# Kernel tuning notes

Hardware: AMD Instinct MI355X
Metric: run time of the kernel (lower is better)

Reference implementation:

```python
import jax, jax.numpy as jnp
import numpy as np

DIM = 1024
HEADS = 16
HDIM = DIM // HEADS
HIDDEN = 4 * DIM
SCALE = HDIM ** -0.5


def layernorm(x, g, b, eps=1e-5):
    mu = jnp.mean(x, axis=-1, keepdims=True)
    var = jnp.var(x, axis=-1, keepdims=True)
    return (x - mu) * jax.lax.rsqrt(var + eps) * g + b


def setup_inputs() -> dict:
    key = jax.random.key(0)
    ks = jax.random.split(key, 8)
    s = 0.02
    return {
        "x": jax.random.normal(ks[0], (4, 1024, DIM), dtype=jnp.float32),
        "ln1_g": jnp.ones((DIM,), jnp.float32),
        "ln1_b": jnp.zeros((DIM,), jnp.float32),
        "ln2_g": jnp.ones((DIM,), jnp.float32),
        "ln2_b": jnp.zeros((DIM,), jnp.float32),
        "qkv_w": jax.random.normal(ks[1], (DIM, 3 * DIM), jnp.float32) * s,
        "qkv_b": jnp.zeros((3 * DIM,), jnp.float32),
        "proj_w": jax.random.normal(ks[2], (DIM, DIM), jnp.float32) * s,
        "proj_b": jnp.zeros((DIM,), jnp.float32),
        "fc1_w": jax.random.normal(ks[3], (DIM, HIDDEN), jnp.float32) * s,
        "fc1_b": jnp.zeros((HIDDEN,), jnp.float32),
        "fc2_w": jax.random.normal(ks[4], (HIDDEN, DIM), jnp.float32) * s,
        "fc2_b": jnp.zeros((DIM,), jnp.float32),
    }


def reference(x, ln1_g, ln1_b, ln2_g, ln2_b, qkv_w, qkv_b, proj_w, proj_b,
              fc1_w, fc1_b, fc2_w, fc2_b):
    B, N, C = x.shape
    # --- attention branch ---
    h = layernorm(x, ln1_g, ln1_b)
    qkv = h @ qkv_w + qkv_b                       # [B,N,3C]
    qkv = qkv.reshape(B, N, 3, HEADS, HDIM)
    q, k, v = jnp.moveaxis(qkv, 2, 0)             # each [B,N,H,Dh]
    q = jnp.swapaxes(q, 1, 2)                      # [B,H,N,Dh]
    k = jnp.swapaxes(k, 1, 2)
    v = jnp.swapaxes(v, 1, 2)
    attn = jnp.einsum('bhqd,bhkd->bhqk', q, k) * SCALE
    attn = jax.nn.softmax(attn, axis=-1)
    o = jnp.einsum('bhqk,bhkd->bhqd', attn, v)     # [B,H,N,Dh]
    o = jnp.swapaxes(o, 1, 2).reshape(B, N, C)
    x = x + (o @ proj_w + proj_b)
    # --- MLP branch ---
    h = layernorm(x, ln2_g, ln2_b)
    h = jax.nn.gelu(h @ fc1_w + fc1_b, approximate=False)
    x = x + (h @ fc2_w + fc2_b)
    return x
```

## Files before the change

kernel.cpp:

```cpp
#include <hip/hip_runtime.h>
#include <math.h>

#define DIM    1024
#define HEADS  16
#define HDIM   64
#define HIDDEN 4096
#define BATCH  4
#define SEQ    1024
#define ROWS   (BATCH * SEQ)

typedef short s16x8 __attribute__((ext_vector_type(8)));
typedef float f32x4 __attribute__((ext_vector_type(4)));

__device__ __forceinline__ float blo(unsigned int u) {
    union { unsigned int i; float f; } x; x.i = u << 16; return x.f;
}
__device__ __forceinline__ float bhi(unsigned int u) {
    union { unsigned int i; float f; } x; x.i = u & 0xffff0000u; return x.f;
}
__device__ __forceinline__ unsigned short f2b(float f) {
    union { float f; unsigned int i; } x; x.f = f;
    unsigned int r = x.i + 0x7fffu + ((x.i >> 16) & 1u);
    return (unsigned short)(r >> 16);
}

__device__ __forceinline__ float gelu_f(float x) {
    float z  = fabsf(x) * 0.70710678118f;
    float t  = __builtin_amdgcn_rcpf(__builtin_fmaf(0.3275911f, z, 1.0f));
    float p  = ((((1.061405429f * t - 1.453152027f) * t + 1.421413741f) * t
                 - 0.284496736f) * t + 0.254829592f) * t;
    float e  = exp2f(-0.72134752f * x * x);
    float w  = 0.5f * p * e;
    float phi = (x >= 0.0f) ? (1.0f - w) : w;
    return x * phi;
}

__device__ __forceinline__ size_t tidx(int row, int k, int Kdim) {
    return ((size_t)(row >> 4) * (Kdim >> 5) + (k >> 5)) * 512
         + (size_t)(((k & 31) >> 3) * 128 + (row & 15) * 8 + (k & 7));
}

__device__ __forceinline__ void gload_lds16(const void* g, void* l) {
    __builtin_amdgcn_global_load_lds(
        (const __attribute__((address_space(1))) unsigned int*)g,
        (__attribute__((address_space(3))) unsigned int*)l, 16, 0, 0);
}

__global__ __launch_bounds__(256) void ln_kernel(const float* __restrict__ x,
                                                 const float* __restrict__ g,
                                                 const float* __restrict__ b,
                                                 unsigned short* __restrict__ out) {
    int row = blockIdx.x;
    const float* xr = x + (size_t)row * DIM;
    int t = threadIdx.x;
    float4 v = *((const float4*)(xr + t * 4));
    float s  = v.x + v.y + v.z + v.w;
    float ss = v.x * v.x + v.y * v.y + v.z * v.z + v.w * v.w;
    __shared__ float red1[256], red2[256];
    red1[t] = s; red2[t] = ss;
    __syncthreads();
    for (int off = 128; off > 0; off >>= 1) {
        if (t < off) { red1[t] += red1[t + off]; red2[t] += red2[t + off]; }
        __syncthreads();
    }
    float mu   = red1[0] * (1.0f / DIM);
    float var  = red2[0] * (1.0f / DIM) - mu * mu;
    float rstd = rsqrtf(var + 1e-5f);
    float4 gv = *((const float4*)(g + t * 4));
    float4 bv = *((const float4*)(b + t * 4));
    ushort4 o;
    o.x = f2b((v.x - mu) * rstd * gv.x + bv.x);
    o.y = f2b((v.y - mu) * rstd * gv.y + bv.y);
    o.z = f2b((v.z - mu) * rstd * gv.z + bv.z);
    o.w = f2b((v.w - mu) * rstd * gv.w + bv.w);
    *((ushort4*)(out + tidx(row, t * 4, DIM))) = o;
}

__global__ __launch_bounds__(256) void reduce_ln(const unsigned short* __restrict__ p0,
                                                 const unsigned short* __restrict__ p1,
                                                 const float* __restrict__ x,
                                                 const float* __restrict__ bias,
                                                 const float* __restrict__ g,
                                                 const float* __restrict__ b,
                                                 float* __restrict__ xout,
                                                 unsigned short* __restrict__ lnout) {
    int row = blockIdx.x;
    int t = threadIdx.x;
    size_t i = (size_t)row * DIM + t * 4;
    float4 xv = *((const float4*)(x + i));
    float4 bi = *((const float4*)(bias + t * 4));
    uint2 w0 = *((const uint2*)(p0 + i));
    uint2 w1 = *((const uint2*)(p1 + i));
    float4 v;
    v.x = xv.x + bi.x + blo(w0.x) + blo(w1.x);
    v.y = xv.y + bi.y + bhi(w0.x) + bhi(w1.x);
    v.z = xv.z + bi.z + blo(w0.y) + blo(w1.y);
    v.w = xv.w + bi.w + bhi(w0.y) + bhi(w1.y);
    *((float4*)(xout + i)) = v;

    float s  = v.x + v.y + v.z + v.w;
    float ss = v.x * v.x + v.y * v.y + v.z * v.z + v.w * v.w;
    __shared__ float red1[256], red2[256];
    red1[t] = s; red2[t] = ss;
    __syncthreads();
    for (int off = 128; off > 0; off >>= 1) {
        if (t < off) { red1[t] += red1[t + off]; red2[t] += red2[t + off]; }
        __syncthreads();
    }
    float mu   = red1[0] * (1.0f / DIM);
    float var  = red2[0] * (1.0f / DIM) - mu * mu;
    float rstd = rsqrtf(var + 1e-5f);
    float4 gv = *((const float4*)(g + t * 4));
    float4 bv = *((const float4*)(b + t * 4));
    ushort4 o;
    o.x = f2b((v.x - mu) * rstd * gv.x + bv.x);
    o.y = f2b((v.y - mu) * rstd * gv.y + bv.y);
    o.z = f2b((v.z - mu) * rstd * gv.z + bv.z);
    o.w = f2b((v.w - mu) * rstd * gv.w + bv.w);
    *((ushort4*)(lnout + tidx(row, t * 4, DIM))) = o;
}

__global__ __launch_bounds__(256) void wconv_t(const float* __restrict__ W,
                                               unsigned short* __restrict__ Wt,
                                               int K, int N) {
    __shared__ unsigned short T[64][68];
    int t = threadIdx.x;
    int n0 = blockIdx.x * 64, k0 = blockIdx.y * 64;
    int cr = t >> 4;
    int cc = (t & 15) * 4;
    #pragma unroll
    for (int r = 0; r < 4; ++r) {
        int kk = cr + 16 * r;
        float4 v = *((const float4*)(W + (size_t)(k0 + kk) * N + n0 + cc));
        T[cc + 0][kk] = f2b(v.x);
        T[cc + 1][kk] = f2b(v.y);
        T[cc + 2][kk] = f2b(v.z);
        T[cc + 3][kk] = f2b(v.w);
    }
    __syncthreads();
    {
        int nn = t >> 2;
        int kg = (t & 3) * 16;
        #pragma unroll
        for (int p = 0; p < 2; ++p) {
            int k8 = kg + p * 8;
            ushort4 lo = *((ushort4*)&T[nn][k8]);
            ushort4 hi = *((ushort4*)&T[nn][k8 + 4]);
            unsigned short* dst = Wt + tidx(n0 + nn, k0 + k8, K);
            *((ushort4*)dst)       = lo;
            *((ushort4*)(dst + 4)) = hi;
        }
    }
}

__global__ __launch_bounds__(256, 4) void mfma_gemm(const unsigned short* __restrict__ A,
                                                 const unsigned short* __restrict__ Bt,
                                                 const float* __restrict__ bias,
                                                 const float* __restrict__ add,
                                                 void* __restrict__ Cout,
                                                 unsigned short* __restrict__ vt,
                                                 unsigned short* __restrict__ p0,
                                                 unsigned short* __restrict__ p1,
                                                 unsigned short* __restrict__ p2,
                                                 unsigned short* __restrict__ p3,
                                                 int M, int N, int K, int Ksplit, int fuse) {
    __shared__ __align__(16) short Asm[8192];
    __shared__ __align__(16) short Bsm[8192];

    const int tid  = threadIdx.x;
    const int lane = tid & 63;
    const int wave = tid >> 6;
    const int wy = wave >> 1, wx = wave & 1;
    const int lr = lane & 15;
    const int lq = lane >> 4;

    int m_t, n_t;
    {
        const int mt = gridDim.x, ntl = gridDim.y, G = 8;
        if (ntl > G) {
            int lin = blockIdx.y * mt + blockIdx.x;
            int gsz = mt * G;
            int grp = lin / gsz;
            int rem = lin - grp * gsz;
            m_t = rem % mt;
            n_t = grp * G + rem / mt;
        } else { m_t = blockIdx.x; n_t = blockIdx.y; }
    }
    const int m0 = m_t * 128, n0 = n_t * 128;
    const int kbase = blockIdx.z * Ksplit;
    const int kch = K >> 5;

    f32x4 acc[4][4];
    #pragma unroll
    for (int i = 0; i < 4; ++i)
        #pragma unroll
        for (int j = 0; j < 4; ++j)
            acc[i][j] = (f32x4){0.f, 0.f, 0.f, 0.f};

    const unsigned short* ag[4]; const unsigned short* bg[4];
    short* al[4]; short* bl[4];
    #pragma unroll
    for (int j = 0; j < 4; ++j) {
        int cid = wave * 4 + j;
        int mb  = cid >> 1;
        int kc  = cid & 1;
        ag[j] = A  + ((size_t)((m0 >> 4) + mb) * kch + (kbase >> 5) + kc) * 512 + lane * 8;
        bg[j] = Bt + ((size_t)((n0 >> 4) + mb) * kch + (kbase >> 5) + kc) * 512 + lane * 8;
        al[j] = &Asm[cid * 512];
        bl[j] = &Bsm[cid * 512];
    }

    for (int k0 = 0; k0 < Ksplit; k0 += 64) {
        #pragma unroll
        for (int j = 0; j < 4; ++j) {
            gload_lds16(ag[j], al[j]);
            gload_lds16(bg[j], bl[j]);
            ag[j] += 1024; bg[j] += 1024;
        }
        __syncthreads();
        #pragma unroll
        for (int kc = 0; kc < 2; ++kc) {
            s16x8 af[4], bf[4];
            #pragma unroll
            for (int i = 0; i < 4; ++i)
                af[i] = *((const s16x8*)&Asm[((wy * 4 + i) * 2 + kc) * 512 + lane * 8]);
            #pragma unroll
            for (int j = 0; j < 4; ++j)
                bf[j] = *((const s16x8*)&Bsm[((wx * 4 + j) * 2 + kc) * 512 + lane * 8]);
            #pragma unroll
            for (int i = 0; i < 4; ++i)
                #pragma unroll
                for (int j = 0; j < 4; ++j)
                    acc[i][j] = __builtin_amdgcn_mfma_f32_16x16x32_bf16(af[i], bf[j], acc[i][j], 0, 0, 0);
        }
        __syncthreads();
    }

    unsigned short* P = nullptr;
    if (fuse == 3) {
        int z = blockIdx.z;
        P = (z == 0) ? p0 : (z == 1) ? p1 : (z == 2) ? p2 : p3;
    }

    #pragma unroll
    for (int j = 0; j < 4; ++j) {
        int col = n0 + wx * 64 + j * 16 + lr;
        float bi = (fuse == 3) ? 0.f : bias[col];
        #pragma unroll
        for (int i = 0; i < 4; ++i) {
            int row0 = m0 + wy * 64 + i * 16 + lq * 4;
            #pragma unroll
            for (int r = 0; r < 4; ++r) {
                float val = acc[i][j][r] + bi;
                int row = row0 + r;
                if (fuse == 3) {
                    P[(size_t)row * N + col] = f2b(val);
                } else if (fuse == 2) {
                    size_t idx = (size_t)row * N + col;
                    ((float*)Cout)[idx] = val + add[idx];
                } else {
                    if (fuse == 1)
                        val = gelu_f(val);
                    unsigned short hv = f2b(val);
                    if (fuse == 0 && vt && col >= 2 * DIM) {
                        int b_ = row >> 10, tok = row & 1023;
                        int hd = col - 2 * DIM, h_ = hd >> 6, d = hd & 63;
                        size_t o = (size_t)(b_ * 16 + h_) * 65536
                                 + ((size_t)(d >> 4) * 32 + (tok >> 5)) * 512
                                 + ((tok & 31) >> 3) * 128 + (d & 15) * 8 + (tok & 7);
                        vt[o] = hv;
                    } else {
                        ((unsigned short*)Cout)[tidx(row, col, N)] = hv;
                    }
                }
            }
        }
    }
}

__global__ __launch_bounds__(256) void reduce_kernel(const unsigned short* __restrict__ p0,
                                                     const unsigned short* __restrict__ p1,
                                                     const unsigned short* __restrict__ p2,
                                                     const unsigned short* __restrict__ p3,
                                                     int S,
                                                     const float* __restrict__ x,
                                                     const float* __restrict__ bias,
                                                     float* __restrict__ out) {
    int i = (blockIdx.x * 256 + threadIdx.x) * 8;
    int col = i & (DIM - 1);
    float4 b0 = *((const float4*)(bias + col));
    float4 b1 = *((const float4*)(bias + col + 4));
    float4 x0 = *((const float4*)(x + i));
    float4 x1 = *((const float4*)(x + i + 4));
    float a[8] = {x0.x + b0.x, x0.y + b0.y, x0.z + b0.z, x0.w + b0.w,
                  x1.x + b1.x, x1.y + b1.y, x1.z + b1.z, x1.w + b1.w};
    const unsigned short* ps[4] = {p0, p1, p2, p3};
    for (int s = 0; s < S; ++s) {
        uint4 w = *((const uint4*)(ps[s] + i));
        a[0] += blo(w.x); a[1] += bhi(w.x);
        a[2] += blo(w.y); a[3] += bhi(w.y);
        a[4] += blo(w.z); a[5] += bhi(w.z);
        a[6] += blo(w.w); a[7] += bhi(w.w);
    }
    *((float4*)(out + i))     = make_float4(a[0], a[1], a[2], a[3]);
    *((float4*)(out + i + 4)) = make_float4(a[4], a[5], a[6], a[7]);
}

__global__ __launch_bounds__(256) void fattn_mfma(const unsigned short* __restrict__ qkv,
                                                  const unsigned short* __restrict__ Vt,
                                                  unsigned short* __restrict__ out) {
    __shared__ __align__(16) short Qs[8192];
    __shared__ __align__(16) short Ks[4096];
    __shared__ __align__(16) short Vs[4096];
    __shared__ __align__(16) short Ps[128 * 72];
    __shared__ __align__(16) short OnesB[512];

    const int tid = threadIdx.x, lane = tid & 63, wave = tid >> 6;
    const int lr = lane & 15, lq = lane >> 4;
    const int L = blockIdx.x;
    const int bh = (L & 7) + 8 * (L >> 6);
    const int b = bh >> 4, h = bh & 15;
    const int q0 = ((L >> 3) & 7) * 128;

    {
        s16x8 z = (s16x8){0,0,0,0,0,0,0,0};
        if (lr == 0) { z[0] = (short)0x3F80; z[1] = (short)0x3F80;
                       z[2] = (short)0x3F80; z[3] = (short)0x3F80;
                       z[4] = (short)0x3F80; z[5] = (short)0x3F80;
                       z[6] = (short)0x3F80; z[7] = (short)0x3F80; }
        if (wave == 0) *((s16x8*)&OnesB[lane * 8]) = z;
    }

    #pragma unroll
    for (int j = 0; j < 4; ++j) {
        int cid = wave * 4 + j;
        const unsigned short* g = qkv + ((size_t)(((b * SEQ + q0) >> 4) + (cid >> 1)) * 96
                                         + 2 * h + (cid & 1)) * 512 + lane * 8;
        gload_lds16(g, &Qs[cid * 512]);
    }

    const unsigned short* kg_[2]; const unsigned short* vg_[2];
    short *kl_[2], *vl_[2];
    #pragma unroll
    for (int j = 0; j < 2; ++j) {
        int cid = wave * 2 + j;
        kg_[j] = qkv + ((size_t)(((b * SEQ) >> 4) + (cid >> 1)) * 96
                        + 32 + 2 * h + (cid & 1)) * 512 + lane * 8;
        vg_[j] = Vt + (size_t)bh * 65536
                 + ((size_t)(cid >> 1) * 32 + (cid & 1)) * 512 + lane * 8;
        kl_[j] = &Ks[cid * 512];
        vl_[j] = &Vs[cid * 512];
    }

    f32x4 osum[2][5];
    #pragma unroll
    for (int i = 0; i < 2; ++i)
        #pragma unroll
        for (int d = 0; d < 5; ++d)
            osum[i][d] = (f32x4){0.f, 0.f, 0.f, 0.f};

    const float c = 0.125f * 1.44269504f;

    for (int k0 = 0; k0 < SEQ; k0 += 64) {
        #pragma unroll
        for (int j = 0; j < 2; ++j) {
            gload_lds16(kg_[j], kl_[j]);
            gload_lds16(vg_[j], vl_[j]);
            kg_[j] += 4 * 96 * 512;
            vg_[j] += 1024;
        }
        __syncthreads();

        f32x4 s[2][4];
        #pragma unroll
        for (int i = 0; i < 2; ++i)
            #pragma unroll
            for (int jb = 0; jb < 4; ++jb)
                s[i][jb] = (f32x4){0.f, 0.f, 0.f, 0.f};
        #pragma unroll
        for (int kc = 0; kc < 2; ++kc) {
            s16x8 aq0 = *((const s16x8*)&Qs[(wave * 4 + 0 + kc) * 512 + lane * 8]);
            s16x8 aq1 = *((const s16x8*)&Qs[(wave * 4 + 2 + kc) * 512 + lane * 8]);
            #pragma unroll
            for (int jb = 0; jb < 4; ++jb) {
                s16x8 bk = *((const s16x8*)&Ks[(jb * 2 + kc) * 512 + lane * 8]);
                s[0][jb] = __builtin_amdgcn_mfma_f32_16x16x32_bf16(aq0, bk, s[0][jb], 0, 0, 0);
                s[1][jb] = __builtin_amdgcn_mfma_f32_16x16x32_bf16(aq1, bk, s[1][jb], 0, 0, 0);
            }
        }

        #pragma unroll
        for (int i = 0; i < 2; ++i)
            #pragma unroll
            for (int r = 0; r < 4; ++r) {
                int prow = (wave * 2 + i) * 16 + lq * 4 + r;
                #pragma unroll
                for (int jb = 0; jb < 4; ++jb)
                    Ps[prow * 72 + jb * 16 + lr] = (short)f2b(exp2f(s[i][jb][r] * c));
            }

        #pragma unroll
        for (int kc = 0; kc < 2; ++kc) {
            s16x8 ap0 = *((const s16x8*)&Ps[((wave * 2 + 0) * 16 + lr) * 72 + kc * 32 + lq * 8]);
            s16x8 ap1 = *((const s16x8*)&Ps[((wave * 2 + 1) * 16 + lr) * 72 + kc * 32 + lq * 8]);
            #pragma unroll
            for (int db = 0; db < 4; ++db) {
                s16x8 bv = *((const s16x8*)&Vs[(db * 2 + kc) * 512 + lane * 8]);
                osum[0][db] = __builtin_amdgcn_mfma_f32_16x16x32_bf16(ap0, bv, osum[0][db], 0, 0, 0);
                osum[1][db] = __builtin_amdgcn_mfma_f32_16x16x32_bf16(ap1, bv, osum[1][db], 0, 0, 0);
            }
            s16x8 bo = *((const s16x8*)&OnesB[lane * 8]);
            osum[0][4] = __builtin_amdgcn_mfma_f32_16x16x32_bf16(ap0, bo, osum[0][4], 0, 0, 0);
            osum[1][4] = __builtin_amdgcn_mfma_f32_16x16x32_bf16(ap1, bo, osum[1][4], 0, 0, 0);
        }
        __syncthreads();
    }

    #pragma unroll
    for (int i = 0; i < 2; ++i) {
        int qrow = q0 + (wave * 2 + i) * 16 + lq * 4;
        #pragma unroll
        for (int r = 0; r < 4; ++r) {
            float lsum = __shfl(osum[i][4][r], lane & 48, 64);
            float inv = 1.0f / lsum;
            int row = b * SEQ + qrow + r;
            #pragma unroll
            for (int db = 0; db < 4; ++db)
                out[tidx(row, h * 64 + db * 16 + lr, DIM)] = f2b(osum[i][db][r] * inv);
        }
    }
}

extern "C" void kernel_launch(void* const* d_in, const int* in_sizes, int n_in,
                              void* d_out, int out_size, void* d_ws, size_t ws_size,
                              hipStream_t stream) {
    const float* x      = (const float*)d_in[0];
    const float* ln1_g  = (const float*)d_in[1];
    const float* ln1_b  = (const float*)d_in[2];
    const float* ln2_g  = (const float*)d_in[3];
    const float* ln2_b  = (const float*)d_in[4];
    const float* qkv_w  = (const float*)d_in[5];
    const float* qkv_b  = (const float*)d_in[6];
    const float* proj_w = (const float*)d_in[7];
    const float* proj_b = (const float*)d_in[8];
    const float* fc1_w  = (const float*)d_in[9];
    const float* fc1_b  = (const float*)d_in[10];
    const float* fc2_w  = (const float*)d_in[11];
    const float* fc2_b  = (const float*)d_in[12];
    float* out = (float*)d_out;

    char* ws = (char*)d_ws;
    unsigned short* wT_fc2  = (unsigned short*)(ws);
    unsigned short* wT_qkv  = (unsigned short*)(ws + (8u  << 20));
    unsigned short* wT_proj = (unsigned short*)(ws + (14u << 20));
    unsigned short* qkvbuf  = (unsigned short*)(ws + (16u << 20));
    unsigned short* Vt      = (unsigned short*)(ws + (40u << 20));
    unsigned short* attnout = (unsigned short*)(ws + (48u << 20));
    unsigned short* lnout   = (unsigned short*)(ws + (56u << 20));
    unsigned short* wT_fc1  = (unsigned short*)(ws + (64u << 20));
    unsigned short* gelu    = (unsigned short*)(ws + (16u << 20));
    unsigned short* pp0 = (unsigned short*)(ws + (16u << 20));
    unsigned short* pp1 = (unsigned short*)(ws + (24u << 20));
    unsigned short* fp0 = (unsigned short*)(ws + (48u << 20));
    unsigned short* fp1 = (unsigned short*)(ws + (56u << 20));
    unsigned short* fp2 = (unsigned short*)(ws + (64u << 20));
    unsigned short* fp3 = (unsigned short*)(ws + (8u  << 20));

    wconv_t<<<dim3(3 * DIM / 64, DIM / 64), 256, 0, stream>>>(qkv_w, wT_qkv, DIM, 3 * DIM);
    wconv_t<<<dim3(DIM / 64, DIM / 64), 256, 0, stream>>>(proj_w, wT_proj, DIM, DIM);
    wconv_t<<<dim3(HIDDEN / 64, DIM / 64), 256, 0, stream>>>(fc1_w, wT_fc1, DIM, HIDDEN);
    wconv_t<<<dim3(DIM / 64, HIDDEN / 64), 256, 0, stream>>>(fc2_w, wT_fc2, HIDDEN, DIM);

    ln_kernel<<<ROWS, 256, 0, stream>>>(x, ln1_g, ln1_b, lnout);
    mfma_gemm<<<dim3(ROWS / 128, 3 * DIM / 128, 1), 256, 0, stream>>>(
        lnout, wT_qkv, qkv_b, nullptr, qkvbuf, Vt, nullptr, nullptr, nullptr, nullptr,
        ROWS, 3 * DIM, DIM, DIM, 0);
    fattn_mfma<<<(SEQ / 128) * BATCH * HEADS, 256, 0, stream>>>(qkvbuf, Vt, attnout);
    mfma_gemm<<<dim3(ROWS / 128, DIM / 128, 2), 256, 0, stream>>>(
        attnout, wT_proj, proj_b, nullptr, nullptr, nullptr, pp0, pp1, nullptr, nullptr,
        ROWS, DIM, DIM, DIM / 2, 3);
    reduce_ln<<<ROWS, 256, 0, stream>>>(pp0, pp1, x, proj_b, ln2_g, ln2_b, out, lnout);
    mfma_gemm<<<dim3(ROWS / 128, HIDDEN / 128, 1), 256, 0, stream>>>(
        lnout, wT_fc1, fc1_b, nullptr, gelu, nullptr, nullptr, nullptr, nullptr, nullptr,
        ROWS, HIDDEN, DIM, DIM, 1);
    mfma_gemm<<<dim3(ROWS / 128, DIM / 128, 4), 256, 0, stream>>>(
        gelu, wT_fc2, fc2_b, nullptr, nullptr, nullptr, fp0, fp1, fp2, fp3,
        ROWS, DIM, HIDDEN, HIDDEN / 4, 3);
    reduce_kernel<<<ROWS * DIM / 2048, 256, 0, stream>>>(
        fp0, fp1, fp2, fp3, 4, out, fc2_b, out);
}
```

Measured before the change: 346.2 us.

## Add 256x256-tile 512-thread pipelined GEMM for QKV, FC1 and FC2

Adds a new bf16 MFMA GEMM kernel with 256x256 output tiles and 8 waves. It double-buffers global-to-LDS loads, interleaved in phases with MFMA compute and explicit vmcnt waits and barriers, and uses an XCD-aware block swizzle. The QKV, FC1 and FC2 launches switch to this kernel to get more operand reuse per tile and overlap memory with compute. The cost is 128KB of LDS per block, very high register pressure (a 32-entry accumulator array), and fewer blocks, for example 64 blocks for the FC2 split-K launch, which may underfill the GPU.

```diff
diff --git a/kernel.cpp b/kernel.cpp
--- a/kernel.cpp
+++ b/kernel.cpp
@@ -278,6 +278,159 @@
     }
 }
 
+__global__ __launch_bounds__(512, 2) void gemm256(const unsigned short* __restrict__ A,
+                                                  const unsigned short* __restrict__ Bt,
+                                                  const float* __restrict__ bias,
+                                                  void* __restrict__ Cout,
+                                                  unsigned short* __restrict__ vt,
+                                                  unsigned short* __restrict__ p0,
+                                                  unsigned short* __restrict__ p1,
+                                                  unsigned short* __restrict__ p2,
+                                                  unsigned short* __restrict__ p3,
+                                                  int M, int N, int K, int Ksplit, int fuse) {
+    __shared__ __align__(16) short As[32768];
+    __shared__ __align__(16) short Bs[32768];
+
+    const int tid  = threadIdx.x;
+    const int lane = tid & 63;
+    const int wave = tid >> 6;
+    const int wy = wave >> 2, wx = wave & 3;
+    const int lr = lane & 15;
+    const int lq = lane >> 4;
+
+    int m_t, n_t;
+    {
+        int gx = gridDim.x;
+        int nwg = gx * gridDim.y;
+        int lin = blockIdx.y * gx + blockIdx.x;
+        if ((nwg & 7) == 0) {
+            int cpx = nwg >> 3;
+            int swz = (lin & 7) * cpx + (lin >> 3);
+            m_t = swz % gx; n_t = swz / gx;
+        } else { m_t = blockIdx.x; n_t = blockIdx.y; }
+    }
+    const int m0 = m_t * 256, n0 = n_t * 256;
+    const int kb = (blockIdx.z * Ksplit) >> 5;
+    const int kch = K >> 5;
+
+    f32x4 acc[8][4];
+    #pragma unroll
+    for (int i = 0; i < 8; ++i)
+        #pragma unroll
+        for (int j = 0; j < 4; ++j)
+            acc[i][j] = (f32x4){0.f, 0.f, 0.f, 0.f};
+
+    const unsigned short* aA = A  + ((size_t)((m0 >> 4) + (wave >> 1)) * kch + kb + (wave & 1)) * 512 + lane * 8;
+    const unsigned short* bB = Bt + ((size_t)((n0 >> 4) + (wave >> 1)) * kch + kb + (wave & 1)) * 512 + lane * 8;
+    short* Asl = As + wave * 512;
+    short* Bsl = Bs + wave * 512;
+
+#define STG_A(buf, t, h) { \
+    gload_lds16(aA + ((size_t)((h) * 8 + 0) * kch + (size_t)(t) * 2) * 512, Asl + ((buf) * 32 + (h) * 16 + 0) * 512); \
+    gload_lds16(aA + ((size_t)((h) * 8 + 4) * kch + (size_t)(t) * 2) * 512, Asl + ((buf) * 32 + (h) * 16 + 8) * 512); }
+#define STG_B(buf, t, h) { \
+    gload_lds16(bB + ((size_t)((h) * 8 + 0) * kch + (size_t)(t) * 2) * 512, Bsl + ((buf) * 32 + (h) * 16 + 0) * 512); \
+    gload_lds16(bB + ((size_t)((h) * 8 + 4) * kch + (size_t)(t) * 2) * 512, Bsl + ((buf) * 32 + (h) * 16 + 8) * 512); }
+#define VMCNT6 asm volatile("s_waitcnt vmcnt(6)" ::: "memory")
+#define VMCNT0 asm volatile("s_waitcnt vmcnt(0)" ::: "memory")
+#define BARRIER asm volatile("s_barrier" ::: "memory")
+
+#define PHASE(buf, q, STAGE_STMT, WAIT_STMT) { \
+    s16x8 af[2][2]; \
+    _Pragma("unroll") for (int s_ = 0; s_ < 2; ++s_) \
+      _Pragma("unroll") for (int kc_ = 0; kc_ < 2; ++kc_) \
+        af[s_][kc_] = *((const s16x8*)&As[((buf) * 32 + ((q) * 4 + wy * 2 + s_) * 2 + kc_) * 512 + lane * 8]); \
+    if ((q) == 0) { \
+      _Pragma("unroll") for (int j_ = 0; j_ < 4; ++j_) \
+        _Pragma("unroll") for (int kc_ = 0; kc_ < 2; ++kc_) \
+          bf[j_][kc_] = *((const s16x8*)&Bs[((buf) * 32 + (wx * 4 + j_) * 2 + kc_) * 512 + lane * 8]); \
+    } \
+    STAGE_STMT; \
+    BARRIER; \
+    __builtin_amdgcn_s_setprio(1); \
+    _Pragma("unroll") for (int kc_ = 0; kc_ < 2; ++kc_) \
+      _Pragma("unroll") for (int s_ = 0; s_ < 2; ++s_) \
+        _Pragma("unroll") for (int j_ = 0; j_ < 4; ++j_) \
+          acc[(q) * 2 + s_][j_] = __builtin_amdgcn_mfma_f32_16x16x32_bf16(af[s_][kc_], bf[j_][kc_], acc[(q) * 2 + s_][j_], 0, 0, 0); \
+    __builtin_amdgcn_s_setprio(0); \
+    WAIT_STMT; \
+    BARRIER; \
+}
+
+    const int NITER = Ksplit >> 7;
+
+    STG_A(0, 0, 0); STG_A(0, 0, 1); STG_B(0, 0, 0); STG_B(0, 0, 1);
+    STG_B(1, 1, 0); STG_B(1, 1, 1); STG_A(1, 1, 0);
+    VMCNT6;
+    BARRIER;
+
+    s16x8 bf[4][2];
+    for (int m = 0; m < NITER - 1; ++m) {
+        const int t = 2 * m;
+        PHASE(0, 0, STG_A(1, t + 1, 1), );
+        PHASE(0, 1, STG_B(0, t + 2, 0), );
+        PHASE(0, 2, STG_B(0, t + 2, 1), );
+        PHASE(0, 3, STG_A(0, t + 2, 0), VMCNT6);
+        PHASE(1, 0, STG_A(0, t + 2, 1), );
+        PHASE(1, 1, STG_B(1, t + 3, 0), );
+        PHASE(1, 2, STG_B(1, t + 3, 1), );
+        PHASE(1, 3, STG_A(1, t + 3, 0), VMCNT6);
+    }
+    {
+        const int tl = 2 * NITER - 1;
+        PHASE(0, 0, STG_A(1, tl, 1), );
+        PHASE(0, 1, , );
+        PHASE(0, 2, , );
+        PHASE(0, 3, , VMCNT0);
+        PHASE(1, 0, , );
+        PHASE(1, 1, , );
+        PHASE(1, 2, , );
+        PHASE(1, 3, , );
+    }
+
+#undef PHASE
+#undef STG_A
+#undef STG_B
+
+    unsigned short* P = nullptr;
+    if (fuse == 3) {
+        int z = blockIdx.z;
+        P = (z == 0) ? p0 : (z == 1) ? p1 : (z == 2) ? p2 : p3;
+    }
+
+    #pragma unroll
+    for (int j = 0; j < 4; ++j) {
+        int col = n0 + (wx * 4 + j) * 16 + lr;
+        float bi = (fuse == 3) ? 0.f : bias[col];
+        #pragma unroll
+        for (int i = 0; i < 8; ++i) {
+            int row0 = m0 + ((i >> 1) * 4 + wy * 2 + (i & 1)) * 16 + lq * 4;
+            #pragma unroll
+            for (int r = 0; r < 4; ++r) {
+                float val = acc[i][j][r] + bi;
+                int row = row0 + r;
+                if (fuse == 3) {
+                    P[(size_t)row * N + col] = f2b(val);
+                } else {
+                    if (fuse == 1)
+                        val = gelu_f(val);
+                    unsigned short hv = f2b(val);
+                    if (fuse == 0 && vt && col >= 2 * DIM) {
+                        int b_ = row >> 10, tok = row & 1023;
+                        int hd = col - 2 * DIM, h_ = hd >> 6, d = hd & 63;
+                        size_t o = (size_t)(b_ * 16 + h_) * 65536
+                                 + ((size_t)(d >> 4) * 32 + (tok >> 5)) * 512
+                                 + ((tok & 31) >> 3) * 128 + (d & 15) * 8 + (tok & 7);
+                        vt[o] = hv;
+                    } else {
+                        ((unsigned short*)Cout)[tidx(row, col, N)] = hv;
+                    }
+                }
+            }
+        }
+    }
+}
+
 __global__ __launch_bounds__(256) void reduce_kernel(const unsigned short* __restrict__ p0,
                                                      const unsigned short* __restrict__ p1,
                                                      const unsigned short* __restrict__ p2,
@@ -472,19 +625,19 @@
     wconv_t<<<dim3(DIM / 64, HIDDEN / 64), 256, 0, stream>>>(fc2_w, wT_fc2, HIDDEN, DIM);
 
     ln_kernel<<<ROWS, 256, 0, stream>>>(x, ln1_g, ln1_b, lnout);
-    mfma_gemm<<<dim3(ROWS / 128, 3 * DIM / 128, 1), 256, 0, stream>>>(
-        lnout, wT_qkv, qkv_b, nullptr, qkvbuf, Vt, nullptr, nullptr, nullptr, nullptr,
+    gemm256<<<dim3(ROWS / 256, 3 * DIM / 256, 1), 512, 0, stream>>>(
+        lnout, wT_qkv, qkv_b, qkvbuf, Vt, nullptr, nullptr, nullptr, nullptr,
         ROWS, 3 * DIM, DIM, DIM, 0);
     fattn_mfma<<<(SEQ / 128) * BATCH * HEADS, 256, 0, stream>>>(qkvbuf, Vt, attnout);
     mfma_gemm<<<dim3(ROWS / 128, DIM / 128, 2), 256, 0, stream>>>(
         attnout, wT_proj, proj_b, nullptr, nullptr, nullptr, pp0, pp1, nullptr, nullptr,
         ROWS, DIM, DIM, DIM / 2, 3);
     reduce_ln<<<ROWS, 256, 0, stream>>>(pp0, pp1, x, proj_b, ln2_g, ln2_b, out, lnout);
-    mfma_gemm<<<dim3(ROWS / 128, HIDDEN / 128, 1), 256, 0, stream>>>(
-        lnout, wT_fc1, fc1_b, nullptr, gelu, nullptr, nullptr, nullptr, nullptr, nullptr,
+    gemm256<<<dim3(ROWS / 256, HIDDEN / 256, 1), 512, 0, stream>>>(
+        lnout, wT_fc1, fc1_b, gelu, nullptr, nullptr, nullptr, nullptr, nullptr,
         ROWS, HIDDEN, DIM, DIM, 1);
-    mfma_gemm<<<dim3(ROWS / 128, DIM / 128, 4), 256, 0, stream>>>(
-        gelu, wT_fc2, fc2_b, nullptr, nullptr, nullptr, fp0, fp1, fp2, fp3,
+    gemm256<<<dim3(ROWS / 256, DIM / 256, 4), 512, 0, stream>>>(
+        gelu, wT_fc2, fc2_b, nullptr, nullptr, fp0, fp1, fp2, fp3,
         ROWS, DIM, HIDDEN, HIDDEN / 4, 3);
     reduce_kernel<<<ROWS * DIM / 2048, 256, 0, stream>>>(
         fp0, fp1, fp2, fp3, 4, out, fc2_b, out);
```

Result: slower. 372.3 us (+7.5%).

## Merge weight conversion with LN1 and stage GEMM epilogue stores through LDS

Applied to the files above, without the earlier changes.

Replaces the four weight-transpose launches and the first layernorm launch with one combined prep kernel that dispatches on block index, cutting launch overhead and letting the small kernels share the GPU. The GEMM epilogue now writes accumulator tiles into the freed LDS (with XOR swizzling) and then emits 16-byte vectorized global stores for both the tiled bf16 output and the split-K partials, replacing scattered 2-byte stores. The unused fp32 add path is removed. The V-transpose path keeps its per-element scatter, and the extra LDS round trip adds work inside the epilogue.

```diff
diff --git a/kernel.cpp b/kernel.cpp
--- a/kernel.cpp
+++ b/kernel.cpp
@@ -46,34 +46,88 @@
         (__attribute__((address_space(3))) unsigned int*)l, 16, 0, 0);
 }
 
-__global__ __launch_bounds__(256) void ln_kernel(const float* __restrict__ x,
-                                                 const float* __restrict__ g,
-                                                 const float* __restrict__ b,
-                                                 unsigned short* __restrict__ out) {
-    int row = blockIdx.x;
-    const float* xr = x + (size_t)row * DIM;
-    int t = threadIdx.x;
-    float4 v = *((const float4*)(xr + t * 4));
-    float s  = v.x + v.y + v.z + v.w;
-    float ss = v.x * v.x + v.y * v.y + v.z * v.z + v.w * v.w;
+__global__ __launch_bounds__(256) void prep_kernel(const float* __restrict__ x,
+                                                   const float* __restrict__ g,
+                                                   const float* __restrict__ b,
+                                                   unsigned short* __restrict__ lnout,
+                                                   const float* __restrict__ qkv_w,
+                                                   unsigned short* __restrict__ wT_qkv,
+                                                   const float* __restrict__ proj_w,
+                                                   unsigned short* __restrict__ wT_proj,
+                                                   const float* __restrict__ fc1_w,
+                                                   unsigned short* __restrict__ wT_fc1,
+                                                   const float* __restrict__ fc2_w,
+                                                   unsigned short* __restrict__ wT_fc2) {
     __shared__ float red1[256], red2[256];
-    red1[t] = s; red2[t] = ss;
-    __syncthreads();
-    for (int off = 128; off > 0; off >>= 1) {
-        if (t < off) { red1[t] += red1[t + off]; red2[t] += red2[t + off]; }
-        __syncthreads();
-    }
-    float mu   = red1[0] * (1.0f / DIM);
-    float var  = red2[0] * (1.0f / DIM) - mu * mu;
-    float rstd = rsqrtf(var + 1e-5f);
-    float4 gv = *((const float4*)(g + t * 4));
-    float4 bv = *((const float4*)(b + t * 4));
-    ushort4 o;
-    o.x = f2b((v.x - mu) * rstd * gv.x + bv.x);
-    o.y = f2b((v.y - mu) * rstd * gv.y + bv.y);
-    o.z = f2b((v.z - mu) * rstd * gv.z + bv.z);
-    o.w = f2b((v.w - mu) * rstd * gv.w + bv.w);
-    *((ushort4*)(out + tidx(row, t * 4, DIM))) = o;
+    __shared__ unsigned short T[64][68];
+    const int bid = blockIdx.x;
+    const int t = threadIdx.x;
+
+    if (bid < ROWS) {
+        int row = bid;
+        const float* xr = x + (size_t)row * DIM;
+        float4 v = *((const float4*)(xr + t * 4));
+        float s  = v.x + v.y + v.z + v.w;
+        float ss = v.x * v.x + v.y * v.y + v.z * v.z + v.w * v.w;
+        red1[t] = s; red2[t] = ss;
+        __syncthreads();
+        for (int off = 128; off > 0; off >>= 1) {
+            if (t < off) { red1[t] += red1[t + off]; red2[t] += red2[t + off]; }
+            __syncthreads();
+        }
+        float mu   = red1[0] * (1.0f / DIM);
+        float var  = red2[0] * (1.0f / DIM) - mu * mu;
+        float rstd = rsqrtf(var + 1e-5f);
+        float4 gv = *((const float4*)(g + t * 4));
+        float4 bv = *((const float4*)(b + t * 4));
+        ushort4 o;
+        o.x = f2b((v.x - mu) * rstd * gv.x + bv.x);
+        o.y = f2b((v.y - mu) * rstd * gv.y + bv.y);
+        o.z = f2b((v.z - mu) * rstd * gv.z + bv.z);
+        o.w = f2b((v.w - mu) * rstd * gv.w + bv.w);
+        *((ushort4*)(lnout + tidx(row, t * 4, DIM))) = o;
+    } else {
+        int tt = bid - ROWS;
+        const float* W; unsigned short* Wt; int K, N, bx, by;
+        if (tt < 768) {
+            W = qkv_w; Wt = wT_qkv; K = DIM; N = 3 * DIM; bx = tt % 48; by = tt / 48;
+        } else if (tt < 768 + 256) {
+            tt -= 768;
+            W = proj_w; Wt = wT_proj; K = DIM; N = DIM; bx = tt % 16; by = tt / 16;
+        } else if (tt < 768 + 256 + 1024) {
+            tt -= 768 + 256;
+            W = fc1_w; Wt = wT_fc1; K = DIM; N = HIDDEN; bx = tt % 64; by = tt / 64;
+        } else {
+            tt -= 768 + 256 + 1024;
+            W = fc2_w; Wt = wT_fc2; K = HIDDEN; N = DIM; bx = tt % 16; by = tt / 16;
+        }
+        int n0 = bx * 64, k0 = by * 64;
+        int cr = t >> 4;
+        int cc = (t & 15) * 4;
+        #pragma unroll
+        for (int r = 0; r < 4; ++r) {
+            int kk = cr + 16 * r;
+            float4 v = *((const float4*)(W + (size_t)(k0 + kk) * N + n0 + cc));
+            T[cc + 0][kk] = f2b(v.x);
+            T[cc + 1][kk] = f2b(v.y);
+            T[cc + 2][kk] = f2b(v.z);
+            T[cc + 3][kk] = f2b(v.w);
+        }
+        __syncthreads();
+        {
+            int nn = t >> 2;
+            int kg = (t & 3) * 16;
+            #pragma unroll
+            for (int p = 0; p < 2; ++p) {
+                int k8 = kg + p * 8;
+                ushort4 lo = *((ushort4*)&T[nn][k8]);
+                ushort4 hi = *((ushort4*)&T[nn][k8 + 4]);
+                unsigned short* dst = Wt + tidx(n0 + nn, k0 + k8, K);
+                *((ushort4*)dst)       = lo;
+                *((ushort4*)(dst + 4)) = hi;
+            }
+        }
+    }
 }
 
 __global__ __launch_bounds__(256) void reduce_ln(const unsigned short* __restrict__ p0,
@@ -120,43 +174,9 @@
     *((ushort4*)(lnout + tidx(row, t * 4, DIM))) = o;
 }
 
-__global__ __launch_bounds__(256) void wconv_t(const float* __restrict__ W,
-                                               unsigned short* __restrict__ Wt,
-                                               int K, int N) {
-    __shared__ unsigned short T[64][68];
-    int t = threadIdx.x;
-    int n0 = blockIdx.x * 64, k0 = blockIdx.y * 64;
-    int cr = t >> 4;
-    int cc = (t & 15) * 4;
-    #pragma unroll
-    for (int r = 0; r < 4; ++r) {
-        int kk = cr + 16 * r;
-        float4 v = *((const float4*)(W + (size_t)(k0 + kk) * N + n0 + cc));
-        T[cc + 0][kk] = f2b(v.x);
-        T[cc + 1][kk] = f2b(v.y);
-        T[cc + 2][kk] = f2b(v.z);
-        T[cc + 3][kk] = f2b(v.w);
-    }
-    __syncthreads();
-    {
-        int nn = t >> 2;
-        int kg = (t & 3) * 16;
-        #pragma unroll
-        for (int p = 0; p < 2; ++p) {
-            int k8 = kg + p * 8;
-            ushort4 lo = *((ushort4*)&T[nn][k8]);
-            ushort4 hi = *((ushort4*)&T[nn][k8 + 4]);
-            unsigned short* dst = Wt + tidx(n0 + nn, k0 + k8, K);
-            *((ushort4*)dst)       = lo;
-            *((ushort4*)(dst + 4)) = hi;
-        }
-    }
-}
-
 __global__ __launch_bounds__(256, 4) void mfma_gemm(const unsigned short* __restrict__ A,
                                                  const unsigned short* __restrict__ Bt,
                                                  const float* __restrict__ bias,
-                                                 const float* __restrict__ add,
                                                  void* __restrict__ Cout,
                                                  unsigned short* __restrict__ vt,
                                                  unsigned short* __restrict__ p0,
@@ -236,44 +256,79 @@
         __syncthreads();
     }
 
-    unsigned short* P = nullptr;
-    if (fuse == 3) {
+    short* Wl = (wave < 2 ? Asm : Bsm) + (wave & 1) * 4096;
+
+    if (fuse == 0 && vt && (n0 + wx * 64) >= 2 * DIM) {
+        #pragma unroll
+        for (int j = 0; j < 4; ++j) {
+            int col = n0 + wx * 64 + j * 16 + lr;
+            float bi = bias[col];
+            #pragma unroll
+            for (int i = 0; i < 4; ++i) {
+                int row0 = m0 + wy * 64 + i * 16 + lq * 4;
+                #pragma unroll
+                for (int r = 0; r < 4; ++r) {
+                    float val = acc[i][j][r] + bi;
+                    int row = row0 + r;
+                    int b_ = row >> 10, tok = row & 1023;
+                    int hd = col - 2 * DIM, h_ = hd >> 6, d = hd & 63;
+                    size_t o = (size_t)(b_ * 16 + h_) * 65536
+                             + ((size_t)(d >> 4) * 32 + (tok >> 5)) * 512
+                             + ((tok & 31) >> 3) * 128 + (d & 15) * 8 + (tok & 7);
+                    vt[o] = f2b(val);
+                }
+            }
+        }
+    } else if (fuse == 3) {
+        #pragma unroll
+        for (int j = 0; j < 4; ++j) {
+            #pragma unroll
+            for (int i = 0; i < 4; ++i) {
+                #pragma unroll
+                for (int r = 0; r < 4; ++r) {
+                    int rowL = i * 16 + lq * 4 + r;
+                    int colL = (j * 16 + lr) ^ ((rowL & 7) << 3);
+                    Wl[rowL * 64 + colL] = (short)f2b(acc[i][j][r]);
+                }
+            }
+        }
         int z = blockIdx.z;
-        P = (z == 0) ? p0 : (z == 1) ? p1 : (z == 2) ? p2 : p3;
-    }
-
-    #pragma unroll
-    for (int j = 0; j < 4; ++j) {
-        int col = n0 + wx * 64 + j * 16 + lr;
-        float bi = (fuse == 3) ? 0.f : bias[col];
-        #pragma unroll
-        for (int i = 0; i < 4; ++i) {
-            int row0 = m0 + wy * 64 + i * 16 + lq * 4;
-            #pragma unroll
-            for (int r = 0; r < 4; ++r) {
-                float val = acc[i][j][r] + bi;
-                int row = row0 + r;
-                if (fuse == 3) {
-                    P[(size_t)row * N + col] = f2b(val);
-                } else if (fuse == 2) {
-                    size_t idx = (size_t)row * N + col;
-                    ((float*)Cout)[idx] = val + add[idx];
-                } else {
-                    if (fuse == 1)
-                        val = gelu_f(val);
-                    unsigned short hv = f2b(val);
-                    if (fuse == 0 && vt && col >= 2 * DIM) {
-                        int b_ = row >> 10, tok = row & 1023;
-                        int hd = col - 2 * DIM, h_ = hd >> 6, d = hd & 63;
-                        size_t o = (size_t)(b_ * 16 + h_) * 65536
-                                 + ((size_t)(d >> 4) * 32 + (tok >> 5)) * 512
-                                 + ((tok & 31) >> 3) * 128 + (d & 15) * 8 + (tok & 7);
-                        vt[o] = hv;
-                    } else {
-                        ((unsigned short*)Cout)[tidx(row, col, N)] = hv;
-                    }
+        unsigned short* P = (z == 0) ? p0 : (z == 1) ? p1 : (z == 2) ? p2 : p3;
+        unsigned short* Prow = P + (size_t)(m0 + wy * 64 + lane) * N + n0 + wx * 64;
+        #pragma unroll
+        for (int c = 0; c < 8; ++c) {
+            int colr = (c * 8) ^ ((lane & 7) << 3);
+            s16x8 v = *((const s16x8*)&Wl[lane * 64 + colr]);
+            *((s16x8*)&Prow[c * 8]) = v;
+        }
+    } else {
+        #pragma unroll
+        for (int j = 0; j < 4; ++j) {
+            float bi = bias[n0 + wx * 64 + j * 16 + lr];
+            #pragma unroll
+            for (int i = 0; i < 4; ++i) {
+                #pragma unroll
+                for (int r = 0; r < 4; ++r) {
+                    float val = acc[i][j][r] + bi;
+                    if (fuse == 1) val = gelu_f(val);
+                    int colL = (j & 1) * 16 + lr;
+                    int hi = colL >> 3;
+                    int pos = hi * 128 + (lq * 4 + r) * 8 + (lr & 7);
+                    pos ^= ((pos >> 7) & 3) << 3;
+                    Wl[(i * 2 + (j >> 1)) * 512 + pos] = (short)f2b(val);
                 }
             }
+        }
+        const size_t rc0 = (size_t)((m0 + wy * 64) >> 4);
+        const size_t cc0 = (size_t)((n0 + wx * 64) >> 5);
+        const size_t nch = (size_t)(N >> 5);
+        #pragma unroll
+        for (int c = 0; c < 8; ++c) {
+            int raddr = lane * 8;
+            raddr ^= ((raddr >> 7) & 3) << 3;
+            s16x8 v = *((const s16x8*)&Wl[c * 512 + raddr]);
+            size_t chunk = (rc0 + (c >> 1)) * nch + cc0 + (c & 1);
+            *((s16x8*)&((unsigned short*)Cout)[chunk * 512 + lane * 8]) = v;
         }
     }
 }
@@ -466,25 +521,22 @@
     unsigned short* fp2 = (unsigned short*)(ws + (64u << 20));
     unsigned short* fp3 = (unsigned short*)(ws + (8u  << 20));
 
-    wconv_t<<<dim3(3 * DIM / 64, DIM / 64), 256, 0, stream>>>(qkv_w, wT_qkv, DIM, 3 * DIM);
-    wconv_t<<<dim3(DIM / 64, DIM / 64), 256, 0, stream>>>(proj_w, wT_proj, DIM, DIM);
-    wconv_t<<<dim3(HIDDEN / 64, DIM / 64), 256, 0, stream>>>(fc1_w, wT_fc1, DIM, HIDDEN);
-    wconv_t<<<dim3(DIM / 64, HIDDEN / 64), 256, 0, stream>>>(fc2_w, wT_fc2, HIDDEN, DIM);
-
-    ln_kernel<<<ROWS, 256, 0, stream>>>(x, ln1_g, ln1_b, lnout);
+    prep_kernel<<<ROWS + 3072, 256, 0, stream>>>(
+        x, ln1_g, ln1_b, lnout,
+        qkv_w, wT_qkv, proj_w, wT_proj, fc1_w, wT_fc1, fc2_w, wT_fc2);
     mfma_gemm<<<dim3(ROWS / 128, 3 * DIM / 128, 1), 256, 0, stream>>>(
-        lnout, wT_qkv, qkv_b, nullptr, qkvbuf, Vt, nullptr, nullptr, nullptr, nullptr,
+        lnout, wT_qkv, qkv_b, qkvbuf, Vt, nullptr, nullptr, nullptr, nullptr,
         ROWS, 3 * DIM, DIM, DIM, 0);
     fattn_mfma<<<(SEQ / 128) * BATCH * HEADS, 256, 0, stream>>>(qkvbuf, Vt, attnout);
     mfma_gemm<<<dim3(ROWS / 128, DIM / 128, 2), 256, 0, stream>>>(
-        attnout, wT_proj, proj_b, nullptr, nullptr, nullptr, pp0, pp1, nullptr, nullptr,
+        attnout, wT_proj, proj_b, nullptr, nullptr, pp0, pp1, nullptr, nullptr,
         ROWS, DIM, DIM, DIM / 2, 3);
     reduce_ln<<<ROWS, 256, 0, stream>>>(pp0, pp1, x, proj_b, ln2_g, ln2_b, out, lnout);
     mfma_gemm<<<dim3(ROWS / 128, HIDDEN / 128, 1), 256, 0, stream>>>(
-        lnout, wT_fc1, fc1_b, nullptr, gelu, nullptr, nullptr, nullptr, nullptr, nullptr,
+        lnout, wT_fc1, fc1_b, gelu, nullptr, nullptr, nullptr, nullptr, nullptr,
         ROWS, HIDDEN, DIM, DIM, 1);
     mfma_gemm<<<dim3(ROWS / 128, DIM / 128, 4), 256, 0, stream>>>(
-        gelu, wT_fc2, fc2_b, nullptr, nullptr, nullptr, fp0, fp1, fp2, fp3,
+        gelu, wT_fc2, fc2_b, nullptr, nullptr, fp0, fp1, fp2, fp3,
         ROWS, DIM, HIDDEN, HIDDEN / 4, 3);
     reduce_kernel<<<ROWS * DIM / 2048, 256, 0, stream>>>(
         fp0, fp1, fp2, fp3, 4, out, fc2_b, out);
```

After: 328.4 us. 1.05x faster.
